# Kernel tuning notes

Measured on AMD Instinct MI355X. Metric: run time of the kernel, lower is better.

## Reference

```python
import jax, jax.numpy as jnp
import numpy as np

LATENT_DIM = 64
CONTEXT_DIM = 128
NUM_LAYERS = 5
NUM_BINS = 8
HIDDEN = 256
TAIL_BOUND = 5.0
MIN_BIN_W = 1e-3
MIN_BIN_H = 1e-3
MIN_DERIV = 1e-3
BATCH = 32768


def setup_inputs() -> dict:
    key = jax.random.key(0)
    ks = jax.random.split(key, 8)
    D, C, L, H = LATENT_DIM, CONTEXT_DIM, NUM_LAYERS, HIDDEN
    out_dim = D * (3 * NUM_BINS - 1)  # 64*23 = 1472
    n_tri = D * (D - 1) // 2  # 2016
    s = 0.05
    return {
        "inputs": jax.random.normal(ks[0], (BATCH, D), jnp.float32) * 2.0,
        "context": jax.random.normal(ks[1], (BATCH, C), jnp.float32),
        "W1": jax.random.normal(ks[2], (L, C, H), jnp.float32) * s,
        "b1": jnp.zeros((L, H), jnp.float32),
        "W2": jax.random.normal(ks[3], (L, H, H), jnp.float32) * s,
        "b2": jnp.zeros((L, H), jnp.float32),
        "W3": jax.random.normal(ks[4], (L, H, out_dim), jnp.float32) * s,
        "b3": jnp.zeros((L, out_dim), jnp.float32),
        "lu_bias": jnp.zeros((L, D), jnp.float32),
        "lower_entries": jax.random.normal(ks[5], (L, n_tri), jnp.float32) * s,
        "upper_entries": jax.random.normal(ks[6], (L, n_tri), jnp.float32) * s,
        "upper_diag": jax.random.normal(ks[7], (L, D), jnp.float32) * s,
    }


def _unconstrained_rqs(x, uw, uh, ud):
    """Rational-quadratic spline with linear tails (nflows semantics).
    x: [B, D]; uw/uh: [B, D, NUM_BINS]; ud: [B, D, NUM_BINS-1].
    Returns (y [B,D], logabsdet [B,D])."""
    Bnd = TAIL_BOUND
    nb = NUM_BINS
    inside = (x >= -Bnd) & (x <= Bnd)
    # pad unnormalized derivatives so boundary derivative == 1
    const = float(np.log(np.exp(1.0 - MIN_DERIV) - 1.0))
    ud = jnp.pad(ud, ((0, 0), (0, 0), (1, 1)), constant_values=const)  # [B,D,nb+1]

    w = jax.nn.softmax(uw, axis=-1)
    w = MIN_BIN_W + (1.0 - MIN_BIN_W * nb) * w
    cumw = jnp.concatenate(
        [jnp.zeros(w.shape[:-1] + (1,), w.dtype), jnp.cumsum(w, axis=-1)], axis=-1)
    cumw = 2.0 * Bnd * cumw - Bnd
    cumw = cumw.at[..., 0].set(-Bnd).at[..., -1].set(Bnd)
    widths = cumw[..., 1:] - cumw[..., :-1]

    h = jax.nn.softmax(uh, axis=-1)
    h = MIN_BIN_H + (1.0 - MIN_BIN_H * nb) * h
    cumh = jnp.concatenate(
        [jnp.zeros(h.shape[:-1] + (1,), h.dtype), jnp.cumsum(h, axis=-1)], axis=-1)
    cumh = 2.0 * Bnd * cumh - Bnd
    cumh = cumh.at[..., 0].set(-Bnd).at[..., -1].set(Bnd)
    heights = cumh[..., 1:] - cumh[..., :-1]

    derivs = MIN_DERIV + jax.nn.softplus(ud)  # [B,D,nb+1]
    delta = heights / widths                  # [B,D,nb]

    xc = jnp.clip(x, -Bnd, Bnd)
    # searchsorted: sum(x >= bin_edges) - 1, clipped to valid bin range
    idx = jnp.clip(jnp.sum(xc[..., None] >= cumw, axis=-1) - 1, 0, nb - 1)[..., None]
    g = lambda a: jnp.take_along_axis(a, idx, axis=-1)[..., 0]

    in_cw = g(cumw)
    in_w = g(widths)
    in_ch = g(cumh)
    in_h = g(heights)
    in_delta = g(delta)
    in_d = g(derivs)
    in_d1 = g(derivs[..., 1:])

    theta = (xc - in_cw) / in_w
    tomt = theta * (1.0 - theta)
    numer = in_h * (in_delta * theta * theta + in_d * tomt)
    denom = in_delta + (in_d + in_d1 - 2.0 * in_delta) * tomt
    out = in_ch + numer / denom
    dnum = in_delta * in_delta * (
        in_d1 * theta * theta + 2.0 * in_delta * tomt + in_d * (1.0 - theta) ** 2)
    ld = jnp.log(dnum) - 2.0 * jnp.log(denom)

    return jnp.where(inside, out, x), jnp.where(inside, ld, 0.0)


def _lu_forward(x, lower_e, upper_e, udiag, bias):
    """nflows LULinear: y = L @ (U @ x) + b, logabsdet = sum(log diag(U))."""
    D = x.shape[-1]
    li = jnp.tril_indices(D, -1)
    ui = jnp.triu_indices(D, 1)
    Lm = jnp.eye(D, dtype=x.dtype).at[li].set(lower_e)
    diag = jax.nn.softplus(udiag) + 1e-3
    Um = jnp.zeros((D, D), x.dtype).at[ui].set(upper_e) + jnp.diag(diag)
    y = x @ Um.T
    y = y @ Lm.T + bias
    return y, jnp.sum(jnp.log(diag))


def reference(inputs, context, W1, b1, W2, b2, W3, b3,
              lu_bias, lower_entries, upper_entries, upper_diag):
    x = inputs
    logdet = jnp.zeros(x.shape[0], x.dtype)
    for l in range(NUM_LAYERS):
        # conditioning net (mask=ones => net sees only context)
        hh = jax.nn.relu(context @ W1[l] + b1[l])
        hh = jax.nn.relu(hh @ W2[l] + b2[l])
        params = (hh @ W3[l] + b3[l]).reshape(x.shape[0], LATENT_DIM, 3 * NUM_BINS - 1)
        uw = params[..., :NUM_BINS]
        uh = params[..., NUM_BINS:2 * NUM_BINS]
        ud = params[..., 2 * NUM_BINS:]
        x, ld = _unconstrained_rqs(x, uw, uh, ud)
        logdet = logdet + jnp.sum(ld, axis=-1)
        x, lld = _lu_forward(x, lower_entries[l], upper_entries[l],
                             upper_diag[l], lu_bias[l])
        logdet = logdet + lld
    base = -0.5 * jnp.sum(x * x, axis=-1) - 0.5 * LATENT_DIM * float(np.log(2.0 * np.pi))
    return base + logdet
```

## Files before the change

kernel.cpp:

```cpp
#include <hip/hip_runtime.h>
#include <hip/hip_bf16.h>
#include <math.h>

#define D 64
#define CDIM 128
#define NL 5
#define NB 8
#define HID 256
#define ODIM 1472
#define PPD 23
#define PPDP 24
#define NPAD 1536
#define NTRI 2016
#define BATCH 32768
#define CHUNK 8192

typedef unsigned short u16;
typedef __attribute__((ext_vector_type(8))) short bf16x8;
typedef __attribute__((ext_vector_type(8))) unsigned short u16x8;
typedef __attribute__((ext_vector_type(4))) float f32x4;
typedef __attribute__((ext_vector_type(8))) float f32x8;

__device__ __forceinline__ float softplusf(float x) {
    return fmaxf(x, 0.0f) + log1pf(__expf(-fabsf(x)));
}
__device__ __forceinline__ float softplus_fast(float x) {
    return fmaxf(x, 0.0f) + __logf(1.0f + __expf(-fabsf(x)));
}
__device__ __forceinline__ float frcp(float x) { return __builtin_amdgcn_rcpf(x); }
__device__ __forceinline__ u16 f2bf(float f) {
    __hip_bfloat16 h = __float2bfloat16(f);
    return *reinterpret_cast<u16*>(&h);
}
__device__ __forceinline__ float bf2f(u16 u) {
    return __uint_as_float(((unsigned int)u) << 16);
}

__device__ __forceinline__ void gload16(const u16* g, const u16* s) {
    __builtin_amdgcn_global_load_lds(
        (const __attribute__((address_space(1))) unsigned int*)(unsigned long long)(uintptr_t)g,
        (__attribute__((address_space(3))) unsigned int*)(unsigned int)(uintptr_t)s,
        16, 0, 0);
}

__device__ __forceinline__ int xcd_swz(int bid, int nwg) {
    int q = nwg >> 3, r = nwg & 7;
    int xcd = bid & 7, idx = bid >> 3;
    return (xcd < r ? xcd * (q + 1) : r * (q + 1) + (xcd - r) * q) + idx;
}

__global__ void cvt_ctx(const float* __restrict__ c, u16* __restrict__ o) {
    int i = blockIdx.x * 256 + threadIdx.x;
    if (i < BATCH * CDIM) o[i] = f2bf(c[i]);
}

__global__ void prep_w12(const float* __restrict__ W1, const float* __restrict__ W2,
                         u16* __restrict__ W1t, u16* __restrict__ W2t) {
    int i = blockIdx.x * 256 + threadIdx.x;
    if (i < NL * HID * CDIM) {
        int k = i % CDIM; int n = (i / CDIM) % HID; int l = i / (CDIM * HID);
        W1t[i] = f2bf(W1[(l * CDIM + k) * HID + n]);
    }
    if (i < NL * HID * HID) {
        int k = i % HID; int n = (i / HID) % HID; int l = i / (HID * HID);
        W2t[i] = f2bf(W2[(l * HID + k) * HID + n]);
    }
}

__global__ void prep_w3(const float* __restrict__ W3, const float* __restrict__ b3,
                        u16* __restrict__ W3t, float* __restrict__ b3p) {
    int i = blockIdx.x * 256 + threadIdx.x;
    if (i < NL * NPAD * HID) {
        int k = i % HID; int n = (i / HID) % NPAD; int l = i / (HID * NPAD);
        int dd = n / PPDP, p = n % PPDP;
        W3t[i] = (p < PPD) ? f2bf(W3[(l * HID + k) * ODIM + dd * PPD + p]) : (u16)0;
    }
    if (i < NL * NPAD) {
        int n = i % NPAD; int l = i / NPAD;
        int dd = n / PPDP, p = n % PPDP;
        b3p[i] = (p < PPD) ? b3[l * ODIM + dd * PPD + p] : 0.0f;
    }
}

__global__ void lu_prep(const float* __restrict__ lower_e,
                        const float* __restrict__ upper_e,
                        const float* __restrict__ udiag,
                        float* __restrict__ At, float* __restrict__ lu_const) {
    int l = blockIdx.x;
    int t = threadIdx.x;
    __shared__ float Ls[D * D];
    __shared__ float Us[D * D];
    __shared__ float red[4];
    for (int idx = t; idx < D * D; idx += 256) {
        int i = idx >> 6, j = idx & 63;
        float lv;
        if (i == j)      lv = 1.0f;
        else if (i > j)  lv = lower_e[l * NTRI + (i * (i - 1)) / 2 + j];
        else             lv = 0.0f;
        Ls[idx] = lv;
        float uv;
        if (i == j)      uv = softplusf(udiag[l * D + i]) + 0.001f;
        else if (j > i)  uv = upper_e[l * NTRI + i * (D - 1) - (i * (i - 1)) / 2 + (j - i - 1)];
        else             uv = 0.0f;
        Us[idx] = uv;
    }
    __syncthreads();
    for (int idx = t; idx < D * D; idx += 256) {
        int i = idx >> 6, j = idx & 63;
        float acc = 0.0f;
        int km = min(i, j);
        for (int k = 0; k <= km; ++k) acc += Ls[i * D + k] * Us[k * D + j];
        At[(l * D + j) * D + i] = acc;
    }
    if (l == 0) {
        float s = 0.0f;
        for (int i = t; i < NL * D; i += 256)
            s += __logf(softplusf(udiag[i]) + 0.001f);
#pragma unroll
        for (int off = 32; off; off >>= 1) s += __shfl_xor(s, off);
        if ((t & 63) == 0) red[t >> 6] = s;
        __syncthreads();
        if (t == 0) lu_const[0] = red[0] + red[1] + red[2] + red[3];
    }
}

__global__ void init_kernel(const float* __restrict__ inp, float* __restrict__ x,
                            float* __restrict__ logdet) {
    int i = blockIdx.x * 256 + threadIdx.x;
    if (i < BATCH * D) x[i] = inp[i];
    if (i < BATCH) logdet[i] = 0.0f;
}

template<int RELU>
__global__ __launch_bounds__(256) void gemm_bf16(
    const u16* __restrict__ A, const u16* __restrict__ Bt,
    const float* __restrict__ bias, u16* __restrict__ Cv,
    int N, int K, int ncol)
{
    __shared__ u16 lds[16384];
    const int t = threadIdx.x;
    const int w = t >> 6, l = t & 63;
    const int wm = w >> 1, wn = w & 1;
    const int wg = xcd_swz(blockIdx.x, gridDim.x);
    const size_t m0 = (size_t)(wg / ncol) * 128;
    const int n0 = (wg % ncol) * 128;
    const int lrow = l & 15, lk = l >> 4;
    const int srow = l >> 3, sslot = l & 7;

    f32x4 acc[4][4] = {};

    for (int k0 = 0; k0 < K; k0 += 64) {
#pragma unroll
        for (int q = 0; q < 4; ++q) {
            int c = q * 4 + w;
            int row = c * 8 + srow;
            int slog = sslot ^ (row & 7);
            gload16(A + (m0 + row) * K + k0 + slog * 8, &lds[c * 512]);
        }
#pragma unroll
        for (int q = 0; q < 4; ++q) {
            int c = q * 4 + w;
            int row = c * 8 + srow;
            int slog = sslot ^ (row & 7);
            gload16(Bt + (size_t)(n0 + row) * K + k0 + slog * 8, &lds[8192 + c * 512]);
        }
        __syncthreads();
#pragma unroll
        for (int ks = 0; ks < 2; ++ks) {
            bf16x8 a[4], b[4];
#pragma unroll
            for (int mf = 0; mf < 4; ++mf) {
                int row = wm * 64 + mf * 16 + lrow;
                int slot = (ks * 4 + lk) ^ (row & 7);
                a[mf] = *(const bf16x8*)&lds[row * 64 + slot * 8];
            }
#pragma unroll
            for (int nf = 0; nf < 4; ++nf) {
                int row = wn * 64 + nf * 16 + lrow;
                int slot = (ks * 4 + lk) ^ (row & 7);
                b[nf] = *(const bf16x8*)&lds[8192 + row * 64 + slot * 8];
            }
#pragma unroll
            for (int mf = 0; mf < 4; ++mf)
#pragma unroll
                for (int nf = 0; nf < 4; ++nf)
                    acc[mf][nf] = __builtin_amdgcn_mfma_f32_16x16x32_bf16(
                        a[mf], b[nf], acc[mf][nf], 0, 0, 0);
        }
        __syncthreads();
    }
#pragma unroll
    for (int nf = 0; nf < 4; ++nf) {
        int col = n0 + wn * 64 + nf * 16 + lrow;
        float bv = bias[col];
#pragma unroll
        for (int mf = 0; mf < 4; ++mf) {
            size_t rbase = m0 + wm * 64 + mf * 16 + lk * 4;
#pragma unroll
            for (int i = 0; i < 4; ++i) {
                float v = acc[mf][nf][i] + bv;
                if (RELU) v = fmaxf(v, 0.0f);
                Cv[(rbase + i) * N + col] = f2bf(v);
            }
        }
    }
}

__device__ __forceinline__ f32x8 cumb(f32x8 p) {
    float m = fmaxf(fmaxf(fmaxf(p[0], p[1]), fmaxf(p[2], p[3])),
                    fmaxf(fmaxf(p[4], p[5]), fmaxf(p[6], p[7])));
    f32x8 e;
    float s = 0.0f;
#pragma unroll
    for (int i = 0; i < 8; ++i) { e[i] = __expf(p[i] - m); s += e[i]; }
    float tt = 0.992f * frcp(s);
    f32x8 c;
    float run = 0.0f;
#pragma unroll
    for (int i = 0; i < 7; ++i) {
        run = fmaf(tt, e[i], run + 0.001f);
        c[i] = fmaf(10.0f, run, -5.0f);
    }
    c[7] = 5.0f;
    return c;
}

__device__ __forceinline__ void rqs_v(float xv, f32x8 uw, f32x8 uh, f32x8 ud,
                                      float& yo, float& ldo) {
    f32x8 cw = cumb(uw);
    f32x8 ch = cumb(uh);
    f32x8 dv;
#pragma unroll
    for (int i = 0; i < 7; ++i) dv[i] = 0.001f + softplus_fast(ud[i]);
    float xc = fminf(fmaxf(xv, -5.0f), 5.0f);
    float icw = -5.0f, icw1 = cw[0], ich = -5.0f, ich1 = ch[0];
    float d0 = 1.0f, d1 = dv[0];
#pragma unroll
    for (int k = 1; k < 8; ++k) {
        bool sel = (xc >= cw[k - 1]);
        icw  = sel ? cw[k - 1] : icw;
        icw1 = sel ? cw[k]     : icw1;
        ich  = sel ? ch[k - 1] : ich;
        ich1 = sel ? ch[k]     : ich1;
        d0   = sel ? dv[k - 1] : d0;
        d1   = sel ? ((k < 7) ? dv[k] : 1.0f) : d1;
    }
    float iw  = icw1 - icw;
    float ih  = ich1 - ich;
    float riw = frcp(iw);
    float dlt = ih * riw;
    float th  = (xc - icw) * riw;
    float omt = 1.0f - th;
    float tomt = th * omt;
    float numer = ih * (dlt * th * th + d0 * tomt);
    float den = dlt + (d0 + d1 - 2.0f * dlt) * tomt;
    float rden = frcp(den);
    float outv = ich + numer * rden;
    float dnum = dlt * dlt * (d1 * th * th + 2.0f * dlt * tomt + d0 * omt * omt);
    float ld = __logf(dnum * rden * rden);
    bool inside = (xv >= -5.0f) && (xv <= 5.0f);
    yo  = inside ? outv : xv;
    ldo = inside ? ld : 0.0f;
}

__global__ __launch_bounds__(512) void spline_lu_kernel(
    const u16* __restrict__ params,
    const float* __restrict__ At, const float* __restrict__ lu_bias,
    float* __restrict__ x, float* __restrict__ logdet,
    int l, int row_base)
{
    __shared__ float y_s[8 * D];
    const int t = threadIdx.x;
    const int d = t & 63, g = t >> 6;
    const size_t crow = (size_t)blockIdx.x * 8 + g;
    const size_t grow = (size_t)row_base + crow;

    const u16x8* pp = (const u16x8*)(params + crow * NPAD + d * PPDP);
    u16x8 q0 = pp[0], q1 = pp[1], q2 = pp[2];
    f32x8 uw, uh, ud;
#pragma unroll
    for (int j = 0; j < 8; ++j) {
        uw[j] = bf2f(q0[j]);
        uh[j] = bf2f(q1[j]);
        ud[j] = bf2f(q2[j]);
    }
    float xv = x[grow * D + d];
    float y, ld;
    rqs_v(xv, uw, uh, ud, y, ld);
    y_s[g * D + d] = y;
#pragma unroll
    for (int off = 32; off; off >>= 1) ld += __shfl_xor(ld, off);
    if (d == 0) logdet[grow] += ld;
    __syncthreads();

    float acc = lu_bias[l * D + d];
    const float* ap = At + (size_t)l * D * D + d;
#pragma unroll 8
    for (int j = 0; j < D; ++j)
        acc = fmaf(y_s[g * D + j], ap[j * D], acc);
    x[grow * D + d] = acc;
}

__global__ void final_kernel(const float* __restrict__ x,
                             const float* __restrict__ logdet,
                             const float* __restrict__ lu_const,
                             float* __restrict__ out) {
    int t = threadIdx.x;
    int b = blockIdx.x * 4 + (t >> 6);
    int d = t & 63;
    float v = x[(size_t)b * D + d];
    float s = v * v;
#pragma unroll
    for (int off = 32; off; off >>= 1) s += __shfl_xor(s, off);
    if (d == 0)
        out[b] = logdet[b] + lu_const[0] - 0.5f * s - 0.5f * 64.0f * 1.8378770664093453f;
}

extern "C" void kernel_launch(void* const* d_in, const int* in_sizes, int n_in,
                              void* d_out, int out_size, void* d_ws, size_t ws_size,
                              hipStream_t stream) {
    const float* inputs  = (const float*)d_in[0];
    const float* context = (const float*)d_in[1];
    const float* W1      = (const float*)d_in[2];
    const float* b1      = (const float*)d_in[3];
    const float* W2      = (const float*)d_in[4];
    const float* b2      = (const float*)d_in[5];
    const float* W3      = (const float*)d_in[6];
    const float* b3      = (const float*)d_in[7];
    const float* lu_bias = (const float*)d_in[8];
    const float* lower_e = (const float*)d_in[9];
    const float* upper_e = (const float*)d_in[10];
    const float* udiag   = (const float*)d_in[11];
    float* out = (float*)d_out;

    char* p = (char*)d_ws;
    auto alloc = [&](size_t bytes) { void* r = p; p += (bytes + 255) & ~(size_t)255; return r; };
    float* x        = (float*)alloc((size_t)BATCH * D * 4);
    float* logdet   = (float*)alloc((size_t)BATCH * 4);
    float* At       = (float*)alloc((size_t)NL * D * D * 4);
    float* lu_const = (float*)alloc(256);
    u16*   ctx_bf   = (u16*)alloc((size_t)BATCH * CDIM * 2);
    u16*   hh1      = (u16*)alloc((size_t)BATCH * HID * 2);
    u16*   hh2      = (u16*)alloc((size_t)BATCH * HID * 2);
    u16*   W1t      = (u16*)alloc((size_t)NL * HID * CDIM * 2);
    u16*   W2t      = (u16*)alloc((size_t)NL * HID * HID * 2);
    u16*   W3t      = (u16*)alloc((size_t)NL * NPAD * HID * 2);
    float* b3p      = (float*)alloc((size_t)NL * NPAD * 4);

    size_t used = (size_t)(p - (char*)d_ws);
    int chunk = (ws_size - used >= (size_t)BATCH * NPAD * 2 + 256) ? BATCH : CHUNK;
    u16* paramsB = (u16*)alloc((size_t)chunk * NPAD * 2);

    cvt_ctx<<<(BATCH * CDIM + 255) / 256, 256, 0, stream>>>(context, ctx_bf);
    prep_w12<<<(NL * HID * HID + 255) / 256, 256, 0, stream>>>(W1, W2, W1t, W2t);
    prep_w3<<<(NL * NPAD * HID + 255) / 256, 256, 0, stream>>>(W3, b3, W3t, b3p);
    lu_prep<<<NL, 256, 0, stream>>>(lower_e, upper_e, udiag, At, lu_const);
    init_kernel<<<(BATCH * D + 255) / 256, 256, 0, stream>>>(inputs, x, logdet);

    for (int l = 0; l < NL; ++l) {
        gemm_bf16<1><<<(BATCH / 128) * 2, 256, 0, stream>>>(
            ctx_bf, W1t + (size_t)l * HID * CDIM, b1 + l * HID, hh1, HID, CDIM, 2);
        gemm_bf16<1><<<(BATCH / 128) * 2, 256, 0, stream>>>(
            hh1, W2t + (size_t)l * HID * HID, b2 + l * HID, hh2, HID, HID, 2);
        for (int c = 0; c < BATCH / chunk; ++c) {
            gemm_bf16<0><<<(chunk / 128) * (NPAD / 128), 256, 0, stream>>>(
                hh2 + (size_t)c * chunk * HID, W3t + (size_t)l * NPAD * HID,
                b3p + l * NPAD, paramsB, NPAD, HID, NPAD / 128);
            spline_lu_kernel<<<chunk / 8, 512, 0, stream>>>(
                paramsB, At, lu_bias, x, logdet, l, c * chunk);
        }
    }
    final_kernel<<<BATCH / 4, 256, 0, stream>>>(x, logdet, lu_const, out);
}
```

Measured before the change: 550.7 us.

## Fuse third conditioning GEMM with spline and LU into one kernel

Replaces the separate W3 GEMM writing bf16 params to global memory followed by the spline/LU kernel with a single fused kernel. Each 512-thread block loads 32 rows of hh2 into LDS, computes the 1472-wide params in four column chunks with MFMA, stages them in LDS, and evaluates the spline per chunk before applying the LU matmul. This removes the global round trip of the large params tensor and the chunking logic. In exchange, W3 fragments are read directly from global/L2 by every block without LDS reuse, and per-block GEMM tiles are small.

```diff
diff --git a/kernel.cpp b/kernel.cpp
--- a/kernel.cpp
+++ b/kernel.cpp
@@ -13,7 +13,12 @@
 #define NPAD 1536
 #define NTRI 2016
 #define BATCH 32768
-#define CHUNK 8192
+
+#define FROWS 32
+#define NCH 4
+#define CPC 384
+#define HPAD 264
+#define PPAD 392
 
 typedef unsigned short u16;
 typedef __attribute__((ext_vector_type(8))) short bf16x8;
@@ -263,42 +268,108 @@
     ldo = inside ? ld : 0.0f;
 }
 
-__global__ __launch_bounds__(512) void spline_lu_kernel(
-    const u16* __restrict__ params,
+__global__ __launch_bounds__(512, 4) void gemm3_spline_lu(
+    const u16* __restrict__ hh2,
+    const u16* __restrict__ W3t,
+    const float* __restrict__ b3p,
     const float* __restrict__ At, const float* __restrict__ lu_bias,
-    float* __restrict__ x, float* __restrict__ logdet,
-    int l, int row_base)
+    float* __restrict__ x, float* __restrict__ logdet, int lay)
 {
-    __shared__ float y_s[8 * D];
+    __shared__ u16 hh2_s[FROWS * HPAD];
+    __shared__ u16 params_s[FROWS * PPAD];
+    __shared__ float y_s[FROWS * 65];
+    __shared__ float ld_s[FROWS];
     const int t = threadIdx.x;
-    const int d = t & 63, g = t >> 6;
-    const size_t crow = (size_t)blockIdx.x * 8 + g;
-    const size_t grow = (size_t)row_base + crow;
-
-    const u16x8* pp = (const u16x8*)(params + crow * NPAD + d * PPDP);
-    u16x8 q0 = pp[0], q1 = pp[1], q2 = pp[2];
-    f32x8 uw, uh, ud;
-#pragma unroll
-    for (int j = 0; j < 8; ++j) {
-        uw[j] = bf2f(q0[j]);
-        uh[j] = bf2f(q1[j]);
-        ud[j] = bf2f(q2[j]);
-    }
-    float xv = x[grow * D + d];
-    float y, ld;
-    rqs_v(xv, uw, uh, ud, y, ld);
-    y_s[g * D + d] = y;
-#pragma unroll
-    for (int off = 32; off; off >>= 1) ld += __shfl_xor(ld, off);
-    if (d == 0) logdet[grow] += ld;
+    const int w = t >> 6;
+    const int ln = t & 63;
+    const int lr = ln & 15, lk = ln >> 4;
+    const int rbase = blockIdx.x * FROWS;
+
+    {
+        int row = t >> 4, k0 = (t & 15) * 16;
+        const u16* src = hh2 + (size_t)(rbase + row) * HID + k0;
+        bf16x8 v0 = *(const bf16x8*)src;
+        bf16x8 v1 = *(const bf16x8*)(src + 8);
+        *(bf16x8*)&hh2_s[row * HPAD + k0] = v0;
+        *(bf16x8*)&hh2_s[row * HPAD + k0 + 8] = v1;
+    }
+    if (t < FROWS) ld_s[t] = 0.0f;
     __syncthreads();
 
-    float acc = lu_bias[l * D + d];
-    const float* ap = At + (size_t)l * D * D + d;
+    float ld_acc = 0.0f;
+    const int sr = t & 31, sd = t >> 5;
+
+    for (int ch = 0; ch < NCH; ++ch) {
+        f32x4 acc[3][2] = {};
+        const u16* wbase = W3t + (size_t)(ch * CPC + w * 48 + lr) * HID + lk * 8;
+#pragma unroll 2
+        for (int ks = 0; ks < 8; ++ks) {
+            bf16x8 hf0 = *(const bf16x8*)&hh2_s[lr * HPAD + ks * 32 + lk * 8];
+            bf16x8 hf1 = *(const bf16x8*)&hh2_s[(16 + lr) * HPAD + ks * 32 + lk * 8];
+#pragma unroll
+            for (int mf = 0; mf < 3; ++mf) {
+                bf16x8 wf = *(const bf16x8*)(wbase + mf * 16 * HID + ks * 32);
+                acc[mf][0] = __builtin_amdgcn_mfma_f32_16x16x32_bf16(wf, hf0, acc[mf][0], 0, 0, 0);
+                acc[mf][1] = __builtin_amdgcn_mfma_f32_16x16x32_bf16(wf, hf1, acc[mf][1], 0, 0, 0);
+            }
+        }
+        __syncthreads();
+
+        {
+            const float* bb = b3p + ch * CPC + w * 48 + 4 * lk;
+#pragma unroll
+            for (int mf = 0; mf < 3; ++mf) {
+                float4 bv = *(const float4*)(bb + mf * 16);
+#pragma unroll
+                for (int rf = 0; rf < 2; ++rf) {
+                    f32x4 v = acc[mf][rf];
+                    unsigned int lo = (unsigned int)f2bf(v[0] + bv.x)
+                                    | ((unsigned int)f2bf(v[1] + bv.y) << 16);
+                    unsigned int hi = (unsigned int)f2bf(v[2] + bv.z)
+                                    | ((unsigned int)f2bf(v[3] + bv.w) << 16);
+                    uint2 pv; pv.x = lo; pv.y = hi;
+                    int r = rf * 16 + lr;
+                    int cbase = w * 48 + mf * 16 + 4 * lk;
+                    *(uint2*)&params_s[r * PPAD + cbase] = pv;
+                }
+            }
+        }
+        __syncthreads();
+
+        {
+            const u16x8* pp = (const u16x8*)&params_s[sr * PPAD + sd * PPDP];
+            u16x8 q0 = pp[0], q1 = pp[1], q2 = pp[2];
+            f32x8 uw, uh, ud;
+#pragma unroll
+            for (int j = 0; j < 8; ++j) {
+                uw[j] = bf2f(q0[j]);
+                uh[j] = bf2f(q1[j]);
+                ud[j] = bf2f(q2[j]);
+            }
+            int dg = ch * 16 + sd;
+            float xv = x[(size_t)(rbase + sr) * D + dg];
+            float y, ldv;
+            rqs_v(xv, uw, uh, ud, y, ldv);
+            y_s[sr * 65 + dg] = y;
+            ld_acc += ldv;
+        }
+    }
+
+    atomicAdd(&ld_s[sr], ld_acc);
+    __syncthreads();
+    if (t < FROWS) logdet[rbase + t] += ld_s[t];
+
+#pragma unroll
+    for (int p = 0; p < 4; ++p) {
+        int idx = p * 512 + t;
+        int r = idx >> 6, i = idx & 63;
+        float acc2 = lu_bias[lay * D + i];
+        const float* ap = At + (size_t)lay * D * D + i;
 #pragma unroll 8
-    for (int j = 0; j < D; ++j)
-        acc = fmaf(y_s[g * D + j], ap[j * D], acc);
-    x[grow * D + d] = acc;
+        for (int j = 0; j < D; ++j)
+            acc2 = fmaf(y_s[r * 65 + j], ap[j * D], acc2);
+        x[(size_t)(rbase + r) * D + i] = acc2;
+    }
 }
 
 __global__ void final_kernel(const float* __restrict__ x,
@@ -347,28 +418,20 @@
     u16*   W3t      = (u16*)alloc((size_t)NL * NPAD * HID * 2);
     float* b3p      = (float*)alloc((size_t)NL * NPAD * 4);
 
-    size_t used = (size_t)(p - (char*)d_ws);
-    int chunk = (ws_size - used >= (size_t)BATCH * NPAD * 2 + 256) ? BATCH : CHUNK;
-    u16* paramsB = (u16*)alloc((size_t)chunk * NPAD * 2);
-
     cvt_ctx<<<(BATCH * CDIM + 255) / 256, 256, 0, stream>>>(context, ctx_bf);
     prep_w12<<<(NL * HID * HID + 255) / 256, 256, 0, stream>>>(W1, W2, W1t, W2t);
     prep_w3<<<(NL * NPAD * HID + 255) / 256, 256, 0, stream>>>(W3, b3, W3t, b3p);
     lu_prep<<<NL, 256, 0, stream>>>(lower_e, upper_e, udiag, At, lu_const);
     init_kernel<<<(BATCH * D + 255) / 256, 256, 0, stream>>>(inputs, x, logdet);
 
-    for (int l = 0; l < NL; ++l) {
+    for (int lay = 0; lay < NL; ++lay) {
         gemm_bf16<1><<<(BATCH / 128) * 2, 256, 0, stream>>>(
-            ctx_bf, W1t + (size_t)l * HID * CDIM, b1 + l * HID, hh1, HID, CDIM, 2);
+            ctx_bf, W1t + (size_t)lay * HID * CDIM, b1 + lay * HID, hh1, HID, CDIM, 2);
         gemm_bf16<1><<<(BATCH / 128) * 2, 256, 0, stream>>>(
-            hh1, W2t + (size_t)l * HID * HID, b2 + l * HID, hh2, HID, HID, 2);
-        for (int c = 0; c < BATCH / chunk; ++c) {
-            gemm_bf16<0><<<(chunk / 128) * (NPAD / 128), 256, 0, stream>>>(
-                hh2 + (size_t)c * chunk * HID, W3t + (size_t)l * NPAD * HID,
-                b3p + l * NPAD, paramsB, NPAD, HID, NPAD / 128);
-            spline_lu_kernel<<<chunk / 8, 512, 0, stream>>>(
-                paramsB, At, lu_bias, x, logdet, l, c * chunk);
-        }
+            hh1, W2t + (size_t)lay * HID * HID, b2 + lay * HID, hh2, HID, HID, 2);
+        gemm3_spline_lu<<<BATCH / FROWS, 512, 0, stream>>>(
+            hh2, W3t + (size_t)lay * NPAD * HID, b3p + (size_t)lay * NPAD,
+            At, lu_bias, x, logdet, lay);
     }
     final_kernel<<<BATCH / 4, 256, 0, stream>>>(x, logdet, lu_const, out);
 }
```

Measured after the change: 744.1 us. 1.35x slower.

## Batch conditioning-net GEMMs across all layers via grid.y layer index

Applied to the files above, without the earlier changes.

Adds per-layer stride arguments to the bf16 GEMM and uses blockIdx.y as the layer index. The first two MLP GEMMs for all five layers now run as one launch each, and when workspace allows, the third GEMM for all layers also runs in one launch before the per-layer spline kernels. This cuts the number of launches and gives the GPU larger grids to fill it better. In exchange it needs much more workspace (all layers' hidden activations and params) and writes and reads a large params buffer through memory.

```diff
diff --git a/kernel.cpp b/kernel.cpp
--- a/kernel.cpp
+++ b/kernel.cpp
@@ -133,11 +133,16 @@
 
 template<int RELU>
 __global__ __launch_bounds__(256) void gemm_bf16(
-    const u16* __restrict__ A, const u16* __restrict__ Bt,
-    const float* __restrict__ bias, u16* __restrict__ Cv,
-    int N, int K, int ncol)
+    const u16* __restrict__ A0, const u16* __restrict__ Bt0,
+    const float* __restrict__ bias0, u16* __restrict__ Cv0,
+    int N, int K, int ncol, size_t sA, size_t sB, size_t sb, size_t sC)
 {
     __shared__ u16 lds[16384];
+    const int ly = blockIdx.y;
+    const u16* A = A0 + (size_t)ly * sA;
+    const u16* Bt = Bt0 + (size_t)ly * sB;
+    const float* bias = bias0 + (size_t)ly * sb;
+    u16* Cv = Cv0 + (size_t)ly * sC;
     const int t = threadIdx.x;
     const int w = t >> 6, l = t & 63;
     const int wm = w >> 1, wn = w & 1;
@@ -340,16 +345,20 @@
     float* At       = (float*)alloc((size_t)NL * D * D * 4);
     float* lu_const = (float*)alloc(256);
     u16*   ctx_bf   = (u16*)alloc((size_t)BATCH * CDIM * 2);
-    u16*   hh1      = (u16*)alloc((size_t)BATCH * HID * 2);
-    u16*   hh2      = (u16*)alloc((size_t)BATCH * HID * 2);
+    u16*   hh1      = (u16*)alloc((size_t)NL * BATCH * HID * 2);
+    u16*   hh2      = (u16*)alloc((size_t)NL * BATCH * HID * 2);
     u16*   W1t      = (u16*)alloc((size_t)NL * HID * CDIM * 2);
     u16*   W2t      = (u16*)alloc((size_t)NL * HID * HID * 2);
     u16*   W3t      = (u16*)alloc((size_t)NL * NPAD * HID * 2);
     float* b3p      = (float*)alloc((size_t)NL * NPAD * 4);
 
     size_t used = (size_t)(p - (char*)d_ws);
-    int chunk = (ws_size - used >= (size_t)BATCH * NPAD * 2 + 256) ? BATCH : CHUNK;
-    u16* paramsB = (u16*)alloc((size_t)chunk * NPAD * 2);
+    size_t avail = ws_size - used;
+    const size_t perLayer = (size_t)BATCH * NPAD * 2;
+    int mode = (avail >= NL * perLayer + 4096) ? 2
+             : (avail >= perLayer + 4096)      ? 1 : 0;
+    u16* paramsB = (u16*)alloc(mode == 2 ? NL * perLayer : (mode == 1 ? perLayer
+                               : (size_t)CHUNK * NPAD * 2));
 
     cvt_ctx<<<(BATCH * CDIM + 255) / 256, 256, 0, stream>>>(context, ctx_bf);
     prep_w12<<<(NL * HID * HID + 255) / 256, 256, 0, stream>>>(W1, W2, W1t, W2t);
@@ -357,17 +366,34 @@
     lu_prep<<<NL, 256, 0, stream>>>(lower_e, upper_e, udiag, At, lu_const);
     init_kernel<<<(BATCH * D + 255) / 256, 256, 0, stream>>>(inputs, x, logdet);
 
-    for (int l = 0; l < NL; ++l) {
-        gemm_bf16<1><<<(BATCH / 128) * 2, 256, 0, stream>>>(
-            ctx_bf, W1t + (size_t)l * HID * CDIM, b1 + l * HID, hh1, HID, CDIM, 2);
-        gemm_bf16<1><<<(BATCH / 128) * 2, 256, 0, stream>>>(
-            hh1, W2t + (size_t)l * HID * HID, b2 + l * HID, hh2, HID, HID, 2);
-        for (int c = 0; c < BATCH / chunk; ++c) {
-            gemm_bf16<0><<<(chunk / 128) * (NPAD / 128), 256, 0, stream>>>(
-                hh2 + (size_t)c * chunk * HID, W3t + (size_t)l * NPAD * HID,
-                b3p + l * NPAD, paramsB, NPAD, HID, NPAD / 128);
-            spline_lu_kernel<<<chunk / 8, 512, 0, stream>>>(
-                paramsB, At, lu_bias, x, logdet, l, c * chunk);
+    dim3 gmlp((BATCH / 128) * 2, NL);
+    gemm_bf16<1><<<gmlp, 256, 0, stream>>>(
+        ctx_bf, W1t, b1, hh1, HID, CDIM, 2,
+        0, (size_t)HID * CDIM, HID, (size_t)BATCH * HID);
+    gemm_bf16<1><<<gmlp, 256, 0, stream>>>(
+        hh1, W2t, b2, hh2, HID, HID, 2,
+        (size_t)BATCH * HID, (size_t)HID * HID, HID, (size_t)BATCH * HID);
+
+    if (mode == 2) {
+        dim3 g3((BATCH / 128) * (NPAD / 128), NL);
+        gemm_bf16<0><<<g3, 256, 0, stream>>>(
+            hh2, W3t, b3p, paramsB, NPAD, HID, NPAD / 128,
+            (size_t)BATCH * HID, (size_t)NPAD * HID, NPAD, (size_t)BATCH * NPAD);
+        for (int l = 0; l < NL; ++l)
+            spline_lu_kernel<<<BATCH / 8, 512, 0, stream>>>(
+                paramsB + (size_t)l * BATCH * NPAD, At, lu_bias, x, logdet, l, 0);
+    } else {
+        int chunk = (mode == 1) ? BATCH : CHUNK;
+        for (int l = 0; l < NL; ++l) {
+            for (int c = 0; c < BATCH / chunk; ++c) {
+                dim3 g3((chunk / 128) * (NPAD / 128), 1);
+                gemm_bf16<0><<<g3, 256, 0, stream>>>(
+                    hh2 + (size_t)l * BATCH * HID + (size_t)c * chunk * HID,
+                    W3t + (size_t)l * NPAD * HID, b3p + (size_t)l * NPAD,
+                    paramsB, NPAD, HID, NPAD / 128, 0, 0, 0, 0);
+                spline_lu_kernel<<<chunk / 8, 512, 0, stream>>>(
+                    paramsB, At, lu_bias, x, logdet, l, c * chunk);
+            }
         }
     }
     final_kernel<<<BATCH / 4, 256, 0, stream>>>(x, logdet, lu_const, out);
```

New measurement: 693.0 us. +25.8%, slower.

## Coalesce weight transposes, vectorize context conversion, stage GEMM epilogue through LDS

Applied to the files above, without the earlier changes.

Replaces the strided-read weight prep kernels with a shared-memory tiled transpose for W1, W2 and W3 (W3 including the padding map), and splits out the b3 prep. The context conversion now reads float4 and writes packed bf16 pairs. The GEMM epilogue packs bf16 pairs with a lane shuffle into a swizzled LDS region per wave, then writes 16-byte coalesced row stores instead of scattered 2-byte stores. The aim is to cut uncoalesced global traffic in the prep kernels and in the GEMM output, which matters most for the large params buffer. The cost is extra LDS traffic, and it relies on each wave's 4096-element LDS region not overlapping operand data still in use.

```diff
diff --git a/kernel.cpp b/kernel.cpp
--- a/kernel.cpp
+++ b/kernel.cpp
@@ -51,30 +51,45 @@
 
 __global__ void cvt_ctx(const float* __restrict__ c, u16* __restrict__ o) {
     int i = blockIdx.x * 256 + threadIdx.x;
-    if (i < BATCH * CDIM) o[i] = f2bf(c[i]);
-}
-
-__global__ void prep_w12(const float* __restrict__ W1, const float* __restrict__ W2,
-                         u16* __restrict__ W1t, u16* __restrict__ W2t) {
+    if (i < BATCH * CDIM / 4) {
+        float4 v = reinterpret_cast<const float4*>(c)[i];
+        unsigned lo = (unsigned)f2bf(v.x) | ((unsigned)f2bf(v.y) << 16);
+        unsigned hi = (unsigned)f2bf(v.z) | ((unsigned)f2bf(v.w) << 16);
+        uint2 pv; pv.x = lo; pv.y = hi;
+        reinterpret_cast<uint2*>(o)[i] = pv;
+    }
+}
+
+template<int MAP>
+__global__ __launch_bounds__(256) void transpose_prep(
+    const float* __restrict__ in, u16* __restrict__ out, int R, int C, int Cout)
+{
+    __shared__ u16 tile[32][33];
+    const int l = blockIdx.z;
+    const int c0 = blockIdx.x * 32, r0 = blockIdx.y * 32;
+    const int tx = threadIdx.x & 31, ty = threadIdx.x >> 5;
+    const float* inl = in + (size_t)l * R * C;
+#pragma unroll
+    for (int i = 0; i < 4; ++i) {
+        int r = r0 + ty * 4 + i;
+        int cc = c0 + tx;
+        int src = cc;
+        if (MAP) { int dd = cc / PPDP, pp = cc % PPDP; src = (pp < PPD) ? dd * PPD + pp : -1; }
+        u16 v = 0;
+        if (src >= 0) v = f2bf(inl[(size_t)r * C + src]);
+        tile[ty * 4 + i][tx] = v;
+    }
+    __syncthreads();
+    u16* outl = out + (size_t)l * Cout * R;
+#pragma unroll
+    for (int i = 0; i < 4; ++i) {
+        int cc = c0 + ty * 4 + i;
+        outl[(size_t)cc * R + r0 + tx] = tile[tx][ty * 4 + i];
+    }
+}
+
+__global__ void prep_b3(const float* __restrict__ b3, float* __restrict__ b3p) {
     int i = blockIdx.x * 256 + threadIdx.x;
-    if (i < NL * HID * CDIM) {
-        int k = i % CDIM; int n = (i / CDIM) % HID; int l = i / (CDIM * HID);
-        W1t[i] = f2bf(W1[(l * CDIM + k) * HID + n]);
-    }
-    if (i < NL * HID * HID) {
-        int k = i % HID; int n = (i / HID) % HID; int l = i / (HID * HID);
-        W2t[i] = f2bf(W2[(l * HID + k) * HID + n]);
-    }
-}
-
-__global__ void prep_w3(const float* __restrict__ W3, const float* __restrict__ b3,
-                        u16* __restrict__ W3t, float* __restrict__ b3p) {
-    int i = blockIdx.x * 256 + threadIdx.x;
-    if (i < NL * NPAD * HID) {
-        int k = i % HID; int n = (i / HID) % NPAD; int l = i / (HID * NPAD);
-        int dd = n / PPDP, p = n % PPDP;
-        W3t[i] = (p < PPD) ? f2bf(W3[(l * HID + k) * ODIM + dd * PPD + p]) : (u16)0;
-    }
     if (i < NL * NPAD) {
         int n = i % NPAD; int l = i / NPAD;
         int dd = n / PPDP, p = n % PPDP;
@@ -189,19 +204,35 @@
         }
         __syncthreads();
     }
-#pragma unroll
-    for (int nf = 0; nf < 4; ++nf) {
-        int col = n0 + wn * 64 + nf * 16 + lrow;
-        float bv = bias[col];
-#pragma unroll
-        for (int mf = 0; mf < 4; ++mf) {
-            size_t rbase = m0 + wm * 64 + mf * 16 + lk * 4;
-#pragma unroll
-            for (int i = 0; i < 4; ++i) {
-                float v = acc[mf][nf][i] + bv;
-                if (RELU) v = fmaxf(v, 0.0f);
-                Cv[(rbase + i) * N + col] = f2bf(v);
+
+    {
+        u16* region = &lds[w * 4096];
+#pragma unroll
+        for (int nf = 0; nf < 4; ++nf) {
+            float bv = bias[n0 + wn * 64 + nf * 16 + lrow];
+#pragma unroll
+            for (int mf = 0; mf < 4; ++mf) {
+#pragma unroll
+                for (int i = 0; i < 4; ++i) {
+                    float v = acc[mf][nf][i] + bv;
+                    if (RELU) v = fmaxf(v, 0.0f);
+                    unsigned b = (unsigned)f2bf(v);
+                    unsigned o = __shfl_xor(b, 1);
+                    if (!(lrow & 1)) {
+                        int r = mf * 16 + lk * 4 + i;
+                        int slot = (nf << 1) | (lrow >> 3);
+                        int dw = r * 32 + ((slot ^ (r & 7)) << 2) + ((lrow & 7) >> 1);
+                        *reinterpret_cast<unsigned*>(&region[dw * 2]) = b | (o << 16);
+                    }
+                }
             }
+        }
+#pragma unroll
+        for (int s = 0; s < 8; ++s) {
+            int r = s * 8 + (l >> 3);
+            int slot = (l & 7) ^ (r & 7);
+            bf16x8 vv = *(const bf16x8*)&region[r * 64 + slot * 8];
+            *(bf16x8*)(Cv + (m0 + wm * 64 + r) * N + n0 + wn * 64 + 8 * (l & 7)) = vv;
         }
     }
 }
@@ -351,9 +382,14 @@
     int chunk = (ws_size - used >= (size_t)BATCH * NPAD * 2 + 256) ? BATCH : CHUNK;
     u16* paramsB = (u16*)alloc((size_t)chunk * NPAD * 2);
 
-    cvt_ctx<<<(BATCH * CDIM + 255) / 256, 256, 0, stream>>>(context, ctx_bf);
-    prep_w12<<<(NL * HID * HID + 255) / 256, 256, 0, stream>>>(W1, W2, W1t, W2t);
-    prep_w3<<<(NL * NPAD * HID + 255) / 256, 256, 0, stream>>>(W3, b3, W3t, b3p);
+    cvt_ctx<<<(BATCH * CDIM / 4 + 255) / 256, 256, 0, stream>>>(context, ctx_bf);
+    transpose_prep<0><<<dim3(HID / 32, CDIM / 32, NL), 256, 0, stream>>>(
+        W1, W1t, CDIM, HID, HID);
+    transpose_prep<0><<<dim3(HID / 32, HID / 32, NL), 256, 0, stream>>>(
+        W2, W2t, HID, HID, HID);
+    transpose_prep<1><<<dim3(NPAD / 32, HID / 32, NL), 256, 0, stream>>>(
+        W3, W3t, HID, ODIM, NPAD);
+    prep_b3<<<(NL * NPAD + 255) / 256, 256, 0, stream>>>(b3, b3p);
     lu_prep<<<NL, 256, 0, stream>>>(lower_e, upper_e, udiag, At, lu_const);
     init_kernel<<<(BATCH * D + 255) / 256, 256, 0, stream>>>(inputs, x, logdet);
 
```

After: 590.8 us. 7.3% more time.
